# Kernel optimization log

Hardware: AMD Instinct MI355X
Metric: run time of the kernel (lower is better)

Reference implementation:

```python
import jax, jax.numpy as jnp
import numpy as np

B, L, HID, TRANS = 16384, 512, 768, 128


def setup_inputs() -> dict:
    key = jax.random.key(0)
    ks = jax.random.split(key, 12)
    def lin(k, out_d, in_d):
        kw, kb = jax.random.split(k)
        s = 1.0 / np.sqrt(in_d)
        return (jax.random.uniform(kw, (out_d, in_d), jnp.float32, -s, s),
                jax.random.uniform(kb, (out_d,), jnp.float32, -s, s))
    W_text, b_text = lin(ks[0], TRANS, HID)
    W_label, b_label = lin(ks[1], TRANS, HID)
    W0, b0 = lin(ks[2], TRANS, 2 * TRANS)
    W1, b1 = lin(ks[3], TRANS, TRANS)
    W2, b2 = lin(ks[4], 1, TRANS)
    target = jax.random.randint(ks[5], (B, L), 0, 2, jnp.int32)
    # guarantee every sample has at least one positive label (torch.mean on empty would NaN)
    target = target.at[:, 0].set(1)
    return {
        "text_embed": jax.random.normal(ks[6], (B, HID), jnp.float32),
        "label_embed": jax.random.normal(ks[7], (L, HID), jnp.float32),
        "target": target,
        "perm": jax.random.permutation(ks[8], B).astype(jnp.int32),
        "W_text": W_text, "b_text": b_text,
        "W_label": W_label, "b_label": b_label,
        "W0": W0, "b0": b0, "W1": W1, "b1": b1, "W2": W2, "b2": b2,
    }


def _network(t, l, W_text, b_text, W_label, b_label, W0, b0, W1, b1, W2, b2):
    tt = t @ W_text.T + b_text            # [B, trans]
    ll = l @ W_label.T + b_label          # [B, trans]
    h = jnp.concatenate([tt, ll], axis=1)  # [B, 2*trans]
    h = jax.nn.relu(h @ W0.T + b0)
    h = jax.nn.relu(h @ W1.T + b1)
    return h @ W2.T + b2                  # [B, 1]


def reference(text_embed, label_embed, target, perm,
              W_text, b_text, W_label, b_label, W0, b0, W1, b1, W2, b2):
    # variable-length mean pooling of label embeddings selected by the multi-hot target
    mask = target.astype(text_embed.dtype)                 # [B, L]
    counts = jnp.maximum(mask.sum(axis=1, keepdims=True), 1.0)
    label_feature_y = (mask @ label_embed) / counts        # [B, hid]
    negative_text = text_embed[perm]                       # shuffled negatives
    params = (W_text, b_text, W_label, b_label, W0, b0, W1, b1, W2, b2)
    E_joint = -jnp.mean(jax.nn.softplus(-_network(text_embed, label_feature_y, *params)))
    E_marginal = jnp.mean(jax.nn.softplus(_network(negative_text, label_feature_y, *params)))
    return E_marginal - E_joint
```

## Files before the change

### kernel.cpp

```cpp
#include <hip/hip_runtime.h>
#include <math.h>

#define BATCH 16384
#define LBL   512
#define HID   768
#define TR    128

typedef unsigned long long u64;
typedef unsigned short ushort_t;
typedef __attribute__((ext_vector_type(8))) short short8;
typedef __attribute__((ext_vector_type(4))) float f32x4;

__device__ __forceinline__ ushort_t f2bf(float f){
  unsigned u = __builtin_bit_cast(unsigned, f);
  u += 0x7FFFu + ((u >> 16) & 1u);
  return (ushort_t)(u >> 16);
}
__device__ __forceinline__ float bf2f(ushort_t h){
  unsigned u = ((unsigned)h) << 16;
  return __builtin_bit_cast(float, u);
}
__device__ __forceinline__ float softplusf(float x){
  return fmaxf(x, 0.0f) + log1pf(expf(-fabsf(x)));
}
__device__ __forceinline__ void gload_lds16(const void* g, void* l){
  __builtin_amdgcn_global_load_lds((const __attribute__((address_space(1))) void*)g,
                                   (__attribute__((address_space(3))) void*)l, 16, 0, 0);
}

__global__ __launch_bounds__(256) void k_w1(
    const float* __restrict__ W0, const float* __restrict__ Wt, const float* __restrict__ Wl,
    const float* __restrict__ bt, const float* __restrict__ bl, const float* __restrict__ b0,
    const float* __restrict__ W1,
    ushort_t* __restrict__ Msw, ushort_t* __restrict__ Qsw, ushort_t* __restrict__ W1B,
    float* __restrict__ KV, float* __restrict__ ACC){
  __shared__ float sw[TR];
  int bi = blockIdx.x, t = threadIdx.x;
  if (bi < 256){
    int i = bi & 127;
    int isQ = bi >> 7;
    const float* src = isQ ? Wl : Wt;
    ushort_t* dst = isQ ? Qsw : Msw;
    if (t < TR) sw[t] = W0[(size_t)i*256 + isQ*128 + t];
    if (!isQ && t < 128) W1B[i*128 + t] = f2bf(W1[i*128 + t]);
    __syncthreads();
    int c = t;
    float a0 = 0.f, a1 = 0.f, a2 = 0.f;
    #pragma unroll 4
    for (int a = 0; a < 128; a++){
      float w = sw[a];
      const float* r = src + (size_t)a*HID;
      a0 = fmaf(w, r[c], a0);
      a1 = fmaf(w, r[c+256], a1);
      a2 = fmaf(w, r[c+512], a2);
    }
    int c7 = c & 7;
    dst[(((c      )>>3)<<10) + (i<<3) + c7] = f2bf(a0);
    dst[(((c + 256)>>3)<<10) + (i<<3) + c7] = f2bf(a1);
    dst[(((c + 512)>>3)<<10) + (i<<3) + c7] = f2bf(a2);
  } else {
    if (t < TR){
      float s = b0[t];
      const float* r = W0 + (size_t)t*256;
      for (int a = 0; a < 128; a++) s = fmaf(r[a], bt[a], s);
      for (int a = 0; a < 128; a++) s = fmaf(r[128+a], bl[a], s);
      KV[t] = s;
    }
    if (t == 0) ACC[0] = 0.f;
  }
}

__global__ __launch_bounds__(256) void k_phase2(
    const float* __restrict__ labe, const ushort_t* __restrict__ Qsw,
    const int* __restrict__ tgt,
    ushort_t* __restrict__ Gt, u64* __restrict__ bits, float* __restrict__ inv){
  __shared__ __align__(16) ushort_t Bs[2][8192];
  __shared__ __align__(16) ushort_t As[2][16][72];
  int bi = blockIdx.x, tid = threadIdx.x;
  if (bi < 32){
    int lane = tid & 63, wave = tid >> 6;
    int m = lane & 15, q = lane >> 4;
    int l0 = bi * 16;
    int arow = tid >> 4, a4 = (tid & 15) * 4;
    const float* ap = labe + (size_t)(l0 + arow)*HID + a4;

    float4 ra = *(const float4*)ap;
    {
      const char* gb = (const char*)Qsw;
      char* lb = (char*)&Bs[0][0];
      #pragma unroll
      for (int p = 0; p < 4; p++)
        gload_lds16(gb + p*4096 + tid*16, lb + p*4096 + tid*16);
    }
    f32x4 acc[2] = {{0,0,0,0},{0,0,0,0}};
    for (int c = 0; c < 12; c++){
      int buf = c & 1;
      ushort_t* ad = &As[buf][arow][a4];
      ad[0]=f2bf(ra.x); ad[1]=f2bf(ra.y); ad[2]=f2bf(ra.z); ad[3]=f2bf(ra.w);
      __syncthreads();
      if (c < 11){
        ra = *(const float4*)(ap + (c+1)*64);
        const char* gb = (const char*)Qsw + (size_t)(c+1)*16384;
        char* lb = (char*)&Bs[buf^1][0];
        #pragma unroll
        for (int p = 0; p < 4; p++)
          gload_lds16(gb + p*4096 + tid*16, lb + p*4096 + tid*16);
      }
      #pragma unroll
      for (int kcc = 0; kcc < 2; kcc++){
        short8 a = *(const short8*)&As[buf][m][kcc*32 + q*8];
        #pragma unroll
        for (int ct = 0; ct < 2; ct++){
          int col = wave*32 + ct*16 + m;
          short8 b = *(const short8*)&Bs[buf][(kcc*4 + q)*1024 + col*8];
          acc[ct] = __builtin_amdgcn_mfma_f32_16x16x32_bf16(a, b, acc[ct], 0, 0, 0);
        }
      }
    }
    __syncthreads();
    ushort_t (*GTs)[24] = (ushort_t(*)[24])&Bs[0][0];
    #pragma unroll
    for (int ct = 0; ct < 2; ct++){
      int col = wave*32 + ct*16 + m;
      #pragma unroll
      for (int r = 0; r < 4; r++)
        GTs[col][q*4 + r] = f2bf(acc[ct][r]);
    }
    __syncthreads();
    int gi = tid >> 1, loff = (tid & 1) * 8;
    *(short8*)(Gt + (size_t)gi*LBL + l0 + loff) = *(const short8*)&GTs[gi][loff];
  } else {
    int bi2 = bi - 32;
    int w = tid >> 6, lane = tid & 63;
    int b0r = bi2*8 + w*2;
    const int* row0 = tgt + (size_t)b0r*LBL;
    const int* row1 = row0 + LBL;
    int v0[8], v1[8];
    #pragma unroll
    for (int c = 0; c < 8; c++) v0[c] = row0[c*64 + lane];
    #pragma unroll
    for (int c = 0; c < 8; c++) v1[c] = row1[c*64 + lane];
    int c0 = 0, c1 = 0;
    #pragma unroll
    for (int c = 0; c < 8; c++){
      u64 m0 = __ballot(v0[c] != 0);
      u64 m1 = __ballot(v1[c] != 0);
      if (lane == 0){
        bits[(size_t)b0r*8 + c] = m0;       c0 += __popcll(m0);
        bits[(size_t)(b0r+1)*8 + c] = m1;   c1 += __popcll(m1);
      }
    }
    if (lane == 0){
      inv[b0r]   = 1.0f / (float)(c0 < 1 ? 1 : c0);
      inv[b0r+1] = 1.0f / (float)(c1 < 1 ? 1 : c1);
    }
  }
}

__global__ __launch_bounds__(256) void k_u2(const float* __restrict__ T, const ushort_t* __restrict__ Msw,
                                            const float* __restrict__ KV, ushort_t* __restrict__ U){
  __shared__ __align__(16) ushort_t Bs[2][8192];
  __shared__ __align__(16) ushort_t As[2][16][72];
  int tid = threadIdx.x;
  int lane = tid & 63, wave = tid >> 6;
  int m = lane & 15, q = lane >> 4;
  int r0 = blockIdx.x * 16;
  int arow = tid >> 4, a4 = (tid & 15) * 4;
  const float* ap = T + (size_t)(r0 + arow)*HID + a4;

  float4 ra = *(const float4*)ap;
  {
    const char* gb = (const char*)Msw;
    char* lb = (char*)&Bs[0][0];
    #pragma unroll
    for (int p = 0; p < 4; p++)
      gload_lds16(gb + p*4096 + tid*16, lb + p*4096 + tid*16);
  }
  f32x4 acc[2] = {{0,0,0,0},{0,0,0,0}};
  for (int c = 0; c < 12; c++){
    int buf = c & 1;
    ushort_t* ad = &As[buf][arow][a4];
    ad[0]=f2bf(ra.x); ad[1]=f2bf(ra.y); ad[2]=f2bf(ra.z); ad[3]=f2bf(ra.w);
    __syncthreads();
    if (c < 11){
      ra = *(const float4*)(ap + (c+1)*64);
      const char* gb = (const char*)Msw + (size_t)(c+1)*16384;
      char* lb = (char*)&Bs[buf^1][0];
      #pragma unroll
      for (int p = 0; p < 4; p++)
        gload_lds16(gb + p*4096 + tid*16, lb + p*4096 + tid*16);
    }
    #pragma unroll
    for (int kcc = 0; kcc < 2; kcc++){
      short8 a = *(const short8*)&As[buf][m][kcc*32 + q*8];
      #pragma unroll
      for (int ct = 0; ct < 2; ct++){
        int col = wave*32 + ct*16 + m;
        short8 b = *(const short8*)&Bs[buf][(kcc*4 + q)*1024 + col*8];
        acc[ct] = __builtin_amdgcn_mfma_f32_16x16x32_bf16(a, b, acc[ct], 0, 0, 0);
      }
    }
  }
  #pragma unroll
  for (int ct = 0; ct < 2; ct++){
    int col = wave*32 + ct*16 + m;
    float kv = KV[col];
    #pragma unroll
    for (int r = 0; r < 4; r++)
      U[(size_t)(r0 + q*4 + r)*TR + col] = f2bf(acc[ct][r] + kv);
  }
}

__global__ __launch_bounds__(256) void k_fuse(const ushort_t* __restrict__ U, const ushort_t* __restrict__ Gt,
                                              const u64* __restrict__ BITS_, const float* __restrict__ INV,
                                              const int* __restrict__ perm, const ushort_t* __restrict__ W1b,
                                              const float* __restrict__ b1, const float* __restrict__ W2,
                                              const float* __restrict__ b2, float* __restrict__ ACC){
  __shared__ __align__(16) unsigned char bits_s[16*80];
  __shared__ __align__(16) ushort_t h0s[32][136];
  __shared__ float sred[4][2][16][17];
  __shared__ float invs[16];
  __shared__ int   permS[16];

  int tid = threadIdx.x;
  int lane = tid & 63, wave = tid >> 6;
  int m = lane & 15, q = lane >> 4;
  int r0 = blockIdx.x * 16;

  if (tid < 64){
    int row = tid >> 2, seg = tid & 3;
    const int4* src = (const int4*)((const char*)BITS_ + (size_t)(r0+row)*64 + seg*16);
    *(int4*)(bits_s + row*80 + seg*16) = *src;
  } else if (tid < 80){
    invs[tid - 64] = INV[r0 + tid - 64];
  } else if (tid < 96){
    permS[tid - 80] = perm[r0 + tid - 80];
  }
  __syncthreads();

  float up[2][4], un[2][4];
  #pragma unroll
  for (int ct = 0; ct < 2; ct++){
    int col = wave*32 + ct*16 + m;
    #pragma unroll
    for (int r = 0; r < 4; r++){
      int rowl = q*4 + r;
      up[ct][r] = bf2f(U[(size_t)(r0 + rowl)*TR + col]);
      un[ct][r] = bf2f(U[(size_t)permS[rowl]*TR + col]);
    }
  }

  f32x4 accV[2] = {{0,0,0,0},{0,0,0,0}};
  const ushort_t* gp[2];
  #pragma unroll
  for (int ct = 0; ct < 2; ct++)
    gp[ct] = Gt + (size_t)(wave*32 + ct*16 + m)*LBL + q*8;
  short8 bcur[2], bnext[2];
  #pragma unroll
  for (int ct = 0; ct < 2; ct++) bcur[ct] = *(const short8*)(gp[ct]);
  int abase = m*80 + q;
  for (int c = 0; c < 16; c++){
    if (c < 15){
      #pragma unroll
      for (int ct = 0; ct < 2; ct++) bnext[ct] = *(const short8*)(gp[ct] + (c+1)*32);
    }
    unsigned bb = bits_s[abase + c*4];
    short8 a;
    #pragma unroll
    for (int j = 0; j < 8; j++) a[j] = (short)(((bb >> j) & 1u) ? 0x3F80 : 0);
    #pragma unroll
    for (int ct = 0; ct < 2; ct++)
      accV[ct] = __builtin_amdgcn_mfma_f32_16x16x32_bf16(a, bcur[ct], accV[ct], 0, 0, 0);
    #pragma unroll
    for (int ct = 0; ct < 2; ct++) bcur[ct] = bnext[ct];
  }

  #pragma unroll
  for (int ct = 0; ct < 2; ct++){
    int col = wave*32 + ct*16 + m;
    #pragma unroll
    for (int r = 0; r < 4; r++){
      int rowl = q*4 + r;
      float v = accV[ct][r] * invs[rowl];
      h0s[rowl][col]      = f2bf(fmaxf(up[ct][r] + v, 0.f));
      h0s[16 + rowl][col] = f2bf(fmaxf(un[ct][r] + v, 0.f));
    }
  }
  __syncthreads();

  float w2c[2], b1c[2];
  #pragma unroll
  for (int ct = 0; ct < 2; ct++){
    int col = wave*32 + ct*16 + m;
    w2c[ct] = W2[col];
    b1c[ct] = b1[col];
  }
  float b2v = b2[0];

  #pragma unroll
  for (int half = 0; half < 2; half++){
    f32x4 accH[2] = {{0,0,0,0},{0,0,0,0}};
    #pragma unroll
    for (int kc = 0; kc < 4; kc++){
      short8 a = *(const short8*)&h0s[half*16 + m][kc*32 + q*8];
      #pragma unroll
      for (int ct = 0; ct < 2; ct++){
        short8 b = *(const short8*)(W1b + (size_t)(wave*32 + ct*16 + m)*TR + kc*32 + q*8);
        accH[ct] = __builtin_amdgcn_mfma_f32_16x16x32_bf16(a, b, accH[ct], 0, 0, 0);
      }
    }
    #pragma unroll
    for (int r = 0; r < 4; r++){
      float sp = 0.f;
      #pragma unroll
      for (int ct = 0; ct < 2; ct++)
        sp = fmaf(w2c[ct], fmaxf(accH[ct][r] + b1c[ct], 0.f), sp);
      sred[wave][half][q*4 + r][m] = sp;
    }
  }
  __syncthreads();

  if (tid < 32){
    int half = tid >> 4, row = tid & 15;
    float s = b2v;
    #pragma unroll
    for (int wx = 0; wx < 4; wx++)
      #pragma unroll
      for (int n = 0; n < 16; n++) s += sred[wx][half][row][n];
    float val = half ? softplusf(s) : softplusf(-s);
    #pragma unroll
    for (int off = 16; off > 0; off >>= 1) val += __shfl_down(val, off);
    if (tid == 0) atomicAdd(ACC, val);
  }
}

__global__ void k_fin(const float* __restrict__ ACC, float* __restrict__ out){
  out[0] = ACC[0] * (1.0f / (float)BATCH);
}

extern "C" void kernel_launch(void* const* d_in, const int* in_sizes, int n_in,
                              void* d_out, int out_size, void* d_ws, size_t ws_size,
                              hipStream_t stream){
  const float* text = (const float*)d_in[0];
  const float* labe = (const float*)d_in[1];
  const int*   tgt  = (const int*)  d_in[2];
  const int*   perm = (const int*)  d_in[3];
  const float* Wt   = (const float*)d_in[4];
  const float* bt   = (const float*)d_in[5];
  const float* Wl   = (const float*)d_in[6];
  const float* bl   = (const float*)d_in[7];
  const float* W0   = (const float*)d_in[8];
  const float* b0   = (const float*)d_in[9];
  const float* W1   = (const float*)d_in[10];
  const float* b1   = (const float*)d_in[11];
  const float* W2   = (const float*)d_in[12];
  const float* b2   = (const float*)d_in[13];

  char* wsb = (char*)d_ws;
  size_t off = 0;
  auto alloc = [&](size_t bytes){
    size_t r = off;
    off += (bytes + 255) & ~(size_t)255;
    return r;
  };
  ushort_t* MSW = (ushort_t*)(wsb + alloc((size_t)TR*HID*2));
  ushort_t* QSW = (ushort_t*)(wsb + alloc((size_t)TR*HID*2));
  ushort_t* GT  = (ushort_t*)(wsb + alloc((size_t)TR*LBL*2));
  ushort_t* W1B = (ushort_t*)(wsb + alloc((size_t)TR*TR*2));
  float*    KV  = (float*)   (wsb + alloc((size_t)TR*4));
  float*    ACC = (float*)   (wsb + alloc(256));
  u64*      BITS= (u64*)     (wsb + alloc((size_t)BATCH*8*8));
  float*    INV = (float*)   (wsb + alloc((size_t)BATCH*4));
  ushort_t* U   = (ushort_t*)(wsb + alloc((size_t)BATCH*TR*2));
  (void)ws_size; (void)in_sizes; (void)n_in; (void)out_size;

  k_w1    <<<257, 256, 0, stream>>>(W0, Wt, Wl, bt, bl, b0, W1, MSW, QSW, W1B, KV, ACC);
  k_phase2<<<2080, 256, 0, stream>>>(labe, QSW, tgt, GT, BITS, INV);
  k_u2    <<<BATCH/16, 256, 0, stream>>>(text, MSW, KV, U);
  k_fuse  <<<BATCH/16, 256, 0, stream>>>(U, GT, BITS, INV, perm, W1B, b1, W2, b2, ACC);
  k_fin   <<<1, 1, 0, stream>>>(ACC, (float*)d_out);
}
```

Before: 185.3 us.

## Fuse target bitmask into final kernel, merge label and text GEMMs, drop finalize

Moves the target-to-bitmask ballot and count computation from the phase2 kernel into the final fused kernel, so the bits and inverse counts no longer round-trip through global memory. The label projection GEMM and the text projection GEMM now run as one launch, and the finalize kernel is removed by scaling inside the atomic add and zeroing the output in the first kernel. Together these cut the launch count from five to three. The cost is that the final kernel now reads the full int target rows itself, adding latency before its MFMA work. The weight-prep unroll factor is also raised.

```diff
diff --git a/kernel.cpp b/kernel.cpp
--- a/kernel.cpp
+++ b/kernel.cpp
@@ -28,12 +28,12 @@
                                    (__attribute__((address_space(3))) void*)l, 16, 0, 0);
 }
 
-__global__ __launch_bounds__(256) void k_w1(
+__global__ __launch_bounds__(256) void k1(
     const float* __restrict__ W0, const float* __restrict__ Wt, const float* __restrict__ Wl,
     const float* __restrict__ bt, const float* __restrict__ bl, const float* __restrict__ b0,
     const float* __restrict__ W1,
     ushort_t* __restrict__ Msw, ushort_t* __restrict__ Qsw, ushort_t* __restrict__ W1B,
-    float* __restrict__ KV, float* __restrict__ ACC){
+    float* __restrict__ KV, float* __restrict__ out){
   __shared__ float sw[TR];
   int bi = blockIdx.x, t = threadIdx.x;
   if (bi < 256){
@@ -46,7 +46,7 @@
     __syncthreads();
     int c = t;
     float a0 = 0.f, a1 = 0.f, a2 = 0.f;
-    #pragma unroll 4
+    #pragma unroll 8
     for (int a = 0; a < 128; a++){
       float w = sw[a];
       const float* r = src + (size_t)a*HID;
@@ -66,24 +66,25 @@
       for (int a = 0; a < 128; a++) s = fmaf(r[128+a], bl[a], s);
       KV[t] = s;
     }
-    if (t == 0) ACC[0] = 0.f;
-  }
-}
-
-__global__ __launch_bounds__(256) void k_phase2(
+    if (t == 0) out[0] = 0.f;
+  }
+}
+
+__global__ __launch_bounds__(256) void k2(
     const float* __restrict__ labe, const ushort_t* __restrict__ Qsw,
-    const int* __restrict__ tgt,
-    ushort_t* __restrict__ Gt, u64* __restrict__ bits, float* __restrict__ inv){
+    const float* __restrict__ T,    const ushort_t* __restrict__ Msw,
+    const float* __restrict__ KV,
+    ushort_t* __restrict__ Gt, ushort_t* __restrict__ U){
   __shared__ __align__(16) ushort_t Bs[2][8192];
   __shared__ __align__(16) ushort_t As[2][16][72];
   int bi = blockIdx.x, tid = threadIdx.x;
+  int lane = tid & 63, wave = tid >> 6;
+  int m = lane & 15, q = lane >> 4;
+  int arow = tid >> 4, a4 = (tid & 15) * 4;
+
   if (bi < 32){
-    int lane = tid & 63, wave = tid >> 6;
-    int m = lane & 15, q = lane >> 4;
     int l0 = bi * 16;
-    int arow = tid >> 4, a4 = (tid & 15) * 4;
     const float* ap = labe + (size_t)(l0 + arow)*HID + a4;
-
     float4 ra = *(const float4*)ap;
     {
       const char* gb = (const char*)Qsw;
@@ -130,111 +131,84 @@
     int gi = tid >> 1, loff = (tid & 1) * 8;
     *(short8*)(Gt + (size_t)gi*LBL + l0 + loff) = *(const short8*)&GTs[gi][loff];
   } else {
-    int bi2 = bi - 32;
-    int w = tid >> 6, lane = tid & 63;
-    int b0r = bi2*8 + w*2;
-    const int* row0 = tgt + (size_t)b0r*LBL;
-    const int* row1 = row0 + LBL;
-    int v0[8], v1[8];
-    #pragma unroll
-    for (int c = 0; c < 8; c++) v0[c] = row0[c*64 + lane];
-    #pragma unroll
-    for (int c = 0; c < 8; c++) v1[c] = row1[c*64 + lane];
-    int c0 = 0, c1 = 0;
-    #pragma unroll
-    for (int c = 0; c < 8; c++){
-      u64 m0 = __ballot(v0[c] != 0);
-      u64 m1 = __ballot(v1[c] != 0);
-      if (lane == 0){
-        bits[(size_t)b0r*8 + c] = m0;       c0 += __popcll(m0);
-        bits[(size_t)(b0r+1)*8 + c] = m1;   c1 += __popcll(m1);
-      }
-    }
-    if (lane == 0){
-      inv[b0r]   = 1.0f / (float)(c0 < 1 ? 1 : c0);
-      inv[b0r+1] = 1.0f / (float)(c1 < 1 ? 1 : c1);
-    }
-  }
-}
-
-__global__ __launch_bounds__(256) void k_u2(const float* __restrict__ T, const ushort_t* __restrict__ Msw,
-                                            const float* __restrict__ KV, ushort_t* __restrict__ U){
-  __shared__ __align__(16) ushort_t Bs[2][8192];
-  __shared__ __align__(16) ushort_t As[2][16][72];
+    int r0 = (bi - 32) * 16;
+    const float* ap = T + (size_t)(r0 + arow)*HID + a4;
+    float4 ra = *(const float4*)ap;
+    {
+      const char* gb = (const char*)Msw;
+      char* lb = (char*)&Bs[0][0];
+      #pragma unroll
+      for (int p = 0; p < 4; p++)
+        gload_lds16(gb + p*4096 + tid*16, lb + p*4096 + tid*16);
+    }
+    f32x4 acc[2] = {{0,0,0,0},{0,0,0,0}};
+    for (int c = 0; c < 12; c++){
+      int buf = c & 1;
+      ushort_t* ad = &As[buf][arow][a4];
+      ad[0]=f2bf(ra.x); ad[1]=f2bf(ra.y); ad[2]=f2bf(ra.z); ad[3]=f2bf(ra.w);
+      __syncthreads();
+      if (c < 11){
+        ra = *(const float4*)(ap + (c+1)*64);
+        const char* gb = (const char*)Msw + (size_t)(c+1)*16384;
+        char* lb = (char*)&Bs[buf^1][0];
+        #pragma unroll
+        for (int p = 0; p < 4; p++)
+          gload_lds16(gb + p*4096 + tid*16, lb + p*4096 + tid*16);
+      }
+      #pragma unroll
+      for (int kcc = 0; kcc < 2; kcc++){
+        short8 a = *(const short8*)&As[buf][m][kcc*32 + q*8];
+        #pragma unroll
+        for (int ct = 0; ct < 2; ct++){
+          int col = wave*32 + ct*16 + m;
+          short8 b = *(const short8*)&Bs[buf][(kcc*4 + q)*1024 + col*8];
+          acc[ct] = __builtin_amdgcn_mfma_f32_16x16x32_bf16(a, b, acc[ct], 0, 0, 0);
+        }
+      }
+    }
+    #pragma unroll
+    for (int ct = 0; ct < 2; ct++){
+      int col = wave*32 + ct*16 + m;
+      float kv = KV[col];
+      #pragma unroll
+      for (int r = 0; r < 4; r++)
+        U[(size_t)(r0 + q*4 + r)*TR + col] = f2bf(acc[ct][r] + kv);
+    }
+  }
+}
+
+__global__ __launch_bounds__(256) void k3(const ushort_t* __restrict__ U, const ushort_t* __restrict__ Gt,
+                                          const int* __restrict__ tgt, const int* __restrict__ perm,
+                                          const ushort_t* __restrict__ W1b, const float* __restrict__ b1,
+                                          const float* __restrict__ W2, const float* __restrict__ b2,
+                                          float* __restrict__ out){
+  __shared__ __align__(16) u64 bits_s8[16*10];
+  __shared__ __align__(16) ushort_t h0s[32][136];
+  __shared__ float sred[4][2][16][17];
+  __shared__ float invs[16];
+  __shared__ int   permS[16];
+
   int tid = threadIdx.x;
   int lane = tid & 63, wave = tid >> 6;
   int m = lane & 15, q = lane >> 4;
   int r0 = blockIdx.x * 16;
-  int arow = tid >> 4, a4 = (tid & 15) * 4;
-  const float* ap = T + (size_t)(r0 + arow)*HID + a4;
-
-  float4 ra = *(const float4*)ap;
-  {
-    const char* gb = (const char*)Msw;
-    char* lb = (char*)&Bs[0][0];
-    #pragma unroll
-    for (int p = 0; p < 4; p++)
-      gload_lds16(gb + p*4096 + tid*16, lb + p*4096 + tid*16);
-  }
-  f32x4 acc[2] = {{0,0,0,0},{0,0,0,0}};
-  for (int c = 0; c < 12; c++){
-    int buf = c & 1;
-    ushort_t* ad = &As[buf][arow][a4];
-    ad[0]=f2bf(ra.x); ad[1]=f2bf(ra.y); ad[2]=f2bf(ra.z); ad[3]=f2bf(ra.w);
-    __syncthreads();
-    if (c < 11){
-      ra = *(const float4*)(ap + (c+1)*64);
-      const char* gb = (const char*)Msw + (size_t)(c+1)*16384;
-      char* lb = (char*)&Bs[buf^1][0];
-      #pragma unroll
-      for (int p = 0; p < 4; p++)
-        gload_lds16(gb + p*4096 + tid*16, lb + p*4096 + tid*16);
-    }
-    #pragma unroll
-    for (int kcc = 0; kcc < 2; kcc++){
-      short8 a = *(const short8*)&As[buf][m][kcc*32 + q*8];
-      #pragma unroll
-      for (int ct = 0; ct < 2; ct++){
-        int col = wave*32 + ct*16 + m;
-        short8 b = *(const short8*)&Bs[buf][(kcc*4 + q)*1024 + col*8];
-        acc[ct] = __builtin_amdgcn_mfma_f32_16x16x32_bf16(a, b, acc[ct], 0, 0, 0);
-      }
-    }
-  }
-  #pragma unroll
-  for (int ct = 0; ct < 2; ct++){
-    int col = wave*32 + ct*16 + m;
-    float kv = KV[col];
-    #pragma unroll
-    for (int r = 0; r < 4; r++)
-      U[(size_t)(r0 + q*4 + r)*TR + col] = f2bf(acc[ct][r] + kv);
-  }
-}
-
-__global__ __launch_bounds__(256) void k_fuse(const ushort_t* __restrict__ U, const ushort_t* __restrict__ Gt,
-                                              const u64* __restrict__ BITS_, const float* __restrict__ INV,
-                                              const int* __restrict__ perm, const ushort_t* __restrict__ W1b,
-                                              const float* __restrict__ b1, const float* __restrict__ W2,
-                                              const float* __restrict__ b2, float* __restrict__ ACC){
-  __shared__ __align__(16) unsigned char bits_s[16*80];
-  __shared__ __align__(16) ushort_t h0s[32][136];
-  __shared__ float sred[4][2][16][17];
-  __shared__ float invs[16];
-  __shared__ int   permS[16];
-
-  int tid = threadIdx.x;
-  int lane = tid & 63, wave = tid >> 6;
-  int m = lane & 15, q = lane >> 4;
-  int r0 = blockIdx.x * 16;
-
-  if (tid < 64){
-    int row = tid >> 2, seg = tid & 3;
-    const int4* src = (const int4*)((const char*)BITS_ + (size_t)(r0+row)*64 + seg*16);
-    *(int4*)(bits_s + row*80 + seg*16) = *src;
-  } else if (tid < 80){
-    invs[tid - 64] = INV[r0 + tid - 64];
-  } else if (tid < 96){
-    permS[tid - 80] = perm[r0 + tid - 80];
+
+  if (tid < 16) permS[tid] = perm[r0 + tid];
+
+  #pragma unroll
+  for (int rr = 0; rr < 4; rr++){
+    int row = wave*4 + rr;
+    const int* rp = tgt + (size_t)(r0 + row)*LBL;
+    int v[8];
+    #pragma unroll
+    for (int c = 0; c < 8; c++) v[c] = rp[c*64 + lane];
+    int cnt = 0;
+    #pragma unroll
+    for (int c = 0; c < 8; c++){
+      u64 mm = __ballot(v[c] != 0);
+      if (lane == 0){ bits_s8[row*10 + c] = mm; cnt += __popcll(mm); }
+    }
+    if (lane == 0) invs[row] = 1.0f / (float)(cnt < 1 ? 1 : cnt);
   }
   __syncthreads();
 
@@ -250,6 +224,7 @@
     }
   }
 
+  const unsigned char* bits_b = (const unsigned char*)bits_s8;
   f32x4 accV[2] = {{0,0,0,0},{0,0,0,0}};
   const ushort_t* gp[2];
   #pragma unroll
@@ -264,7 +239,7 @@
       #pragma unroll
       for (int ct = 0; ct < 2; ct++) bnext[ct] = *(const short8*)(gp[ct] + (c+1)*32);
     }
-    unsigned bb = bits_s[abase + c*4];
+    unsigned bb = bits_b[abase + c*4];
     short8 a;
     #pragma unroll
     for (int j = 0; j < 8; j++) a[j] = (short)(((bb >> j) & 1u) ? 0x3F80 : 0);
@@ -330,12 +305,8 @@
     float val = half ? softplusf(s) : softplusf(-s);
     #pragma unroll
     for (int off = 16; off > 0; off >>= 1) val += __shfl_down(val, off);
-    if (tid == 0) atomicAdd(ACC, val);
-  }
-}
-
-__global__ void k_fin(const float* __restrict__ ACC, float* __restrict__ out){
-  out[0] = ACC[0] * (1.0f / (float)BATCH);
+    if (tid == 0) atomicAdd(out, val * (1.0f / (float)BATCH));
+  }
 }
 
 extern "C" void kernel_launch(void* const* d_in, const int* in_sizes, int n_in,
@@ -368,15 +339,10 @@
   ushort_t* GT  = (ushort_t*)(wsb + alloc((size_t)TR*LBL*2));
   ushort_t* W1B = (ushort_t*)(wsb + alloc((size_t)TR*TR*2));
   float*    KV  = (float*)   (wsb + alloc((size_t)TR*4));
-  float*    ACC = (float*)   (wsb + alloc(256));
-  u64*      BITS= (u64*)     (wsb + alloc((size_t)BATCH*8*8));
-  float*    INV = (float*)   (wsb + alloc((size_t)BATCH*4));
   ushort_t* U   = (ushort_t*)(wsb + alloc((size_t)BATCH*TR*2));
   (void)ws_size; (void)in_sizes; (void)n_in; (void)out_size;
 
-  k_w1    <<<257, 256, 0, stream>>>(W0, Wt, Wl, bt, bl, b0, W1, MSW, QSW, W1B, KV, ACC);
-  k_phase2<<<2080, 256, 0, stream>>>(labe, QSW, tgt, GT, BITS, INV);
-  k_u2    <<<BATCH/16, 256, 0, stream>>>(text, MSW, KV, U);
-  k_fuse  <<<BATCH/16, 256, 0, stream>>>(U, GT, BITS, INV, perm, W1B, b1, W2, b2, ACC);
-  k_fin   <<<1, 1, 0, stream>>>(ACC, (float*)d_out);
-}
+  k1<<<257, 256, 0, stream>>>(W0, Wt, Wl, bt, bl, b0, W1, MSW, QSW, W1B, KV, (float*)d_out);
+  k2<<<1056, 256, 0, stream>>>(labe, QSW, text, MSW, KV, GT, U);
+  k3<<<BATCH/16, 256, 0, stream>>>(U, GT, tgt, perm, W1B, b1, W2, b2, (float*)d_out);
+}
```

New measurement: 172.8 us. -6.8%, faster.
